# Performance work log

Measured on AMD Instinct MI355X. Metric: run time of the kernel, lower is better.

The kernel has to match this reference:

```python
import jax, jax.numpy as jnp
import numpy as np

H, KV, D, HID = 32, 2, 128, 4096
SQ, SMAX, CP, L = 1024, 4096, 3072, 4
LAYER_IDX = 0


def setup_inputs() -> dict:
    key = jax.random.key(0)
    ks = jax.random.split(key, 14)
    hidden_states = jax.random.normal(ks[0], (1, HID, 1, SQ), jnp.float32)
    # RoPE tables (values in [-1,1]; layout per forward: cos/sin act on last dim of K,
    # cos_t/sin_t are the transposed tables acting on dim -2 of Q)
    cos = jax.random.uniform(ks[1], (1, 1, SQ, D), jnp.float32, -1.0, 1.0)
    sin = jax.random.uniform(ks[2], (1, 1, SQ, D), jnp.float32, -1.0, 1.0)
    cos_t = jax.random.uniform(ks[3], (1, 1, D, SQ), jnp.float32, -1.0, 1.0)
    sin_t = jax.random.uniform(ks[4], (1, 1, D, SQ), jnp.float32, -1.0, 1.0)
    # causal mask in (kv_pos, q_pos) layout: query q sits at absolute position CP+q
    kv_pos = jnp.arange(SMAX)[:, None]
    q_pos = jnp.arange(SQ)[None, :]
    attention_mask = jnp.where(kv_pos <= CP + q_pos, 0.0, -1e9).astype(jnp.float32)[None, None]
    key_cache = jax.random.normal(ks[5], (L, KV, SMAX, D), jnp.float32)
    value_cache = jax.random.normal(ks[6], (L, KV, SMAX, D), jnp.float32)
    s = 0.02
    wq = jax.random.normal(ks[7], (H * D, HID), jnp.float32) * s
    bq = jax.random.normal(ks[8], (H * D,), jnp.float32) * s
    wk = jax.random.normal(ks[9], (KV * D, HID), jnp.float32) * s
    bk = jax.random.normal(ks[10], (KV * D,), jnp.float32) * s
    wv = jax.random.normal(ks[11], (KV * D, HID), jnp.float32) * s
    bv = jax.random.normal(ks[12], (KV * D,), jnp.float32) * s
    wo = jax.random.normal(ks[13], (HID, H * D), jnp.float32) * s
    return dict(hidden_states=hidden_states, cos=cos, sin=sin, cos_t=cos_t, sin_t=sin_t,
                attention_mask=attention_mask, key_cache=key_cache, value_cache=value_cache,
                wq=wq, bq=bq, wk=wk, bk=bk, wv=wv, bv=bv, wo=wo, cache_position=CP)


def _rotate_half(x, axis):
    x1, x2 = jnp.split(x, 2, axis=axis)
    return jnp.concatenate([-x2, x1], axis=axis)


def reference(hidden_states, cos, sin, cos_t, sin_t, attention_mask,
              key_cache, value_cache, wq, bq, wk, bk, wv, bv, wo, cache_position):
    cp = int(cache_position)
    # 1x1-conv projections == matmul over channel dim; hidden_states (1, HID, 1, SQ)
    q = jnp.einsum('oi,bihs->bohs', wq, hidden_states) + bq[None, :, None, None]
    k = jnp.einsum('oi,bihs->bohs', wk, hidden_states) + bk[None, :, None, None]
    v = jnp.einsum('oi,bihs->bohs', wv, hidden_states) + bv[None, :, None, None]
    q = q.reshape(1, H, D, SQ)                      # (1, H, D, Sq)
    k = k.reshape(1, KV, D, SQ).swapaxes(2, 3)      # (1, KV, Sq, D)
    v = v.reshape(1, KV, D, SQ).swapaxes(2, 3)      # (1, KV, Sq, D)
    # split-half RoPE: q rotated along dim -2 (head_dim axis), k along dim -1
    q = q * cos_t + _rotate_half(q, -2) * sin_t
    k = k * cos + _rotate_half(k, -1) * sin
    # scatter into KV cache at [layer_idx, :, cp:cp+SQ]
    kc = key_cache.at[LAYER_IDX, :, cp:cp + SQ, :].set(k[0])
    vc = value_cache.at[LAYER_IDX, :, cp:cp + SQ, :].set(v[0])
    kl = kc[LAYER_IDX]   # (KV, Smax, D)
    vl = vc[LAYER_IDX]   # (KV, Smax, D)
    qg = q.reshape(KV, H // KV, D, SQ)  # group G=H/KV query heads per kv head
    # K @ Q per kv-head group, softmax over kv positions (axis=2)
    attn = jnp.einsum('ksd,kgdq->kgsq', kl, qg) / jnp.sqrt(jnp.float32(D))
    attn = attn + attention_mask[0]     # broadcast (1, Smax, Sq) over (KV, G, Smax, Sq)
    attn = jax.nn.softmax(attn, axis=2)
    out = jnp.einsum('kgsq,ksd->kgqd', attn, vl)    # (KV, G, Sq, D)
    out = out.reshape(1, H, SQ, D).swapaxes(2, 3).reshape(1, H * D, 1, SQ)
    out = jnp.einsum('oi,bihs->bohs', wo, out)      # (1, HID, 1, Sq)
    return out
```

## Files before the change

### kernel.cpp

```cpp
#include <hip/hip_runtime.h>
#include <stdint.h>

#define H_    32
#define KV_   2
#define D_    128
#define HID_  4096
#define SQ_   1024
#define SMAX_ 4096

typedef unsigned short u16;
typedef __attribute__((ext_vector_type(8))) short bf16x8;
typedef __attribute__((ext_vector_type(8))) unsigned short u16x8;
typedef __attribute__((ext_vector_type(4))) float f32x4;

#define MFMA16(a, b, c) __builtin_amdgcn_mfma_f32_16x16x32_bf16(a, b, c, 0, 0, 0)

__device__ __forceinline__ u16 f2bf(float f) {
  unsigned u = __float_as_uint(f);
  u += 0x7fffu + ((u >> 16) & 1u);
  return (u16)(u >> 16);
}
__device__ __forceinline__ float bf2f(u16 u) {
  return __uint_as_float(((unsigned)u) << 16);
}
__device__ __forceinline__ float exp2_fast(float x) {
  float r;
  asm("v_exp_f32 %0, %1" : "=v"(r) : "v"(x));
  return r;
}
__device__ __forceinline__ unsigned cvt_pk_bf16(float lo, float hi) {
  unsigned r;
  asm("v_cvt_pk_bf16_f32 %0, %1, %2" : "=v"(r) : "v"(lo), "v"(hi));
  return r;
}

__device__ __forceinline__ void gl_lds16(const void* g, void* l) {
  __builtin_amdgcn_global_load_lds(
      (const __attribute__((address_space(1))) unsigned int*)g,
      (__attribute__((address_space(3))) unsigned int*)l, 16, 0, 0);
}

__global__ __launch_bounds__(256) void k_ht(const float* __restrict__ hs,
                                            u16* __restrict__ ht) {
  __shared__ float tl[64][65];
  const int i0 = blockIdx.x << 6, s0 = blockIdx.y << 6;
  const int tid = threadIdx.x;
  {
    const int r = tid >> 2, c = (tid & 3) << 4;
    const float* p = hs + (i0 + r) * SQ_ + s0 + c;
    float4 a = *(const float4*)p;
    float4 b = *(const float4*)(p + 4);
    float4 cc = *(const float4*)(p + 8);
    float4 d = *(const float4*)(p + 12);
    float* q = &tl[r][c];
    q[0] = a.x; q[1] = a.y; q[2] = a.z; q[3] = a.w;
    q[4] = b.x; q[5] = b.y; q[6] = b.z; q[7] = b.w;
    q[8] = cc.x; q[9] = cc.y; q[10] = cc.z; q[11] = cc.w;
    q[12] = d.x; q[13] = d.y; q[14] = d.z; q[15] = d.w;
  }
  __syncthreads();
  {
    const int sr = tid >> 2, c = (tid & 3) << 4;
    u16x8 o0, o1;
#pragma unroll
    for (int j = 0; j < 8; ++j) o0[j] = f2bf(tl[c + j][sr]);
#pragma unroll
    for (int j = 0; j < 8; ++j) o1[j] = f2bf(tl[c + 8 + j][sr]);
    u16* q = ht + (s0 + sr) * HID_ + i0 + c;
    *(u16x8*)q = o0;
    *(u16x8*)(q + 8) = o1;
  }
}

__global__ __launch_bounds__(256) void k_wconv4(const float* __restrict__ s0,
                                                const float* __restrict__ s1,
                                                const float* __restrict__ s2,
                                                const float* __restrict__ s3,
                                                u16* __restrict__ dbase) {
  const int N0 = (H_ * D_ * HID_) / 8;
  const int N1 = (KV_ * D_ * HID_) / 8;
  const int NT = N0 + 2 * N1 + N0;
  const int stride = gridDim.x << 8;
  for (int i = (blockIdx.x << 8) + threadIdx.x; i < NT; i += stride) {
    const float* s;
    int j;
    if (i < N0) { s = s0; j = i; }
    else if (i < N0 + N1) { s = s1; j = i - N0; }
    else if (i < N0 + 2 * N1) { s = s2; j = i - N0 - N1; }
    else { s = s3; j = i - N0 - 2 * N1; }
    const float4 a = ((const float4*)s)[2 * j];
    const float4 b = ((const float4*)s)[2 * j + 1];
    u16x8 o;
    o[0] = f2bf(a.x); o[1] = f2bf(a.y); o[2] = f2bf(a.z); o[3] = f2bf(a.w);
    o[4] = f2bf(b.x); o[5] = f2bf(b.y); o[6] = f2bf(b.z); o[7] = f2bf(b.w);
    ((u16x8*)dbase)[i] = o;
  }
}

template <int OUTMODE, bool SWZ>
__global__ __launch_bounds__(256, 2) void k_gemm_bf(const u16* __restrict__ A,
                                                    const float* __restrict__ bias,
                                                    const u16* __restrict__ B,
                                                    void* __restrict__ Cout,
                                                    const int* __restrict__ cpp,
                                                    int ldc,
                                                    const float* __restrict__ bk2,
                                                    const float* __restrict__ bv2,
                                                    u16* __restrict__ knr2,
                                                    u16* __restrict__ vt2) {
  __shared__ u16 a_t[2][64 * 64];
  __shared__ u16 b_t[2][128 * 64];
  int nx, my;
  if (SWZ) {
    const int bid = blockIdx.x;
    const int xcd = bid & 7, t = bid >> 3;
    nx = t & 7;
    my = ((t >> 3) << 3) | xcd;
  } else {
    nx = blockIdx.x;
    my = blockIdx.y;
  }
  const int n0 = nx << 7, m0 = my << 6;
  const int tid = threadIdx.x, wid = tid >> 6, lane = tid & 63;
  const int l15 = lane & 15, l4 = lane >> 4;
  const int wn = wid << 5;
  const f32x4 z4 = {0.f, 0.f, 0.f, 0.f};
  f32x4 acc[4][2];
#pragma unroll
  for (int i = 0; i < 4; ++i)
#pragma unroll
    for (int j = 0; j < 2; ++j) acc[i][j] = z4;

  const int lr8 = lane >> 3, sl = lane & 7;
  const char* sp[6];
  u16* dp[6];
  int stp[6];
#pragma unroll
  for (int j = 0; j < 6; ++j) {
    const int L = wid * 6 + j;
    const bool isA = (L < 8);
    const int Lr = isA ? L : (L - 8);
    const int row = (Lr << 3) + lr8;
    const int cs = sl ^ (row & 7);
    const size_t grow = isA ? (size_t)(m0 + row) : (size_t)(n0 + row);
    sp[j] = (const char*)((isA ? A : B) + grow * HID_) + (cs << 4);
    dp[j] = (isA ? &a_t[0][0] : &b_t[0][0]) + (Lr << 9);
    stp[j] = isA ? 4096 : 8192;
  }
#define GSTAGE(buf, kt)                                     \
  {                                                         \
    _Pragma("unroll") for (int j = 0; j < 6; ++j)           \
        gl_lds16(sp[j] + ((size_t)(kt) << 7),               \
                 dp[j] + ((buf) ? stp[j] : 0));             \
  }

  GSTAGE(0, 0);
  __syncthreads();
  int cur = 0;
  for (int kt = 0; kt < HID_ / 64; ++kt) {
    if (kt + 1 < HID_ / 64) GSTAGE(cur ^ 1, kt + 1);
#pragma unroll
    for (int kk = 0; kk < 2; ++kk) {
      bf16x8 af[4], bfr[2];
#pragma unroll
      for (int mf = 0; mf < 4; ++mf) {
        const int row = mf * 16 + l15;
        const int slt = ((kk << 2) + l4) ^ (row & 7);
        af[mf] = *(const bf16x8*)((const char*)&a_t[cur][0] + (row << 7) + (slt << 4));
      }
#pragma unroll
      for (int nf = 0; nf < 2; ++nf) {
        const int row = wn + nf * 16 + l15;
        const int slt = ((kk << 2) + l4) ^ (row & 7);
        bfr[nf] = *(const bf16x8*)((const char*)&b_t[cur][0] + (row << 7) + (slt << 4));
      }
#pragma unroll
      for (int nf = 0; nf < 2; ++nf)
#pragma unroll
        for (int mf = 0; mf < 4; ++mf) acc[mf][nf] = MFMA16(af[mf], bfr[nf], acc[mf][nf]);
    }
    __syncthreads();
    cur ^= 1;
  }
#undef GSTAGE

  if (OUTMODE == 3) {
    const int cp = cpp[0];
#pragma unroll
    for (int mf = 0; mf < 4; ++mf) {
#pragma unroll
      for (int r = 0; r < 4; ++r) {
        const int m = m0 + mf * 16 + (l4 << 2) + r;
        float bi;
        u16* dst;
        if (m < 4096) { bi = bias[m]; dst = (u16*)Cout + (size_t)m * SQ_; }
        else if (m < 4352) { bi = bk2[m - 4096]; dst = knr2 + (size_t)(m - 4096) * SQ_; }
        else { bi = bv2[m - 4352]; dst = vt2 + (size_t)(m - 4352) * SMAX_ + cp; }
#pragma unroll
        for (int nf = 0; nf < 2; ++nf) {
          const int n = n0 + wn + nf * 16 + l15;
          dst[n] = f2bf(acc[mf][nf][r] + bi);
        }
      }
    }
  } else {
#pragma unroll
    for (int mf = 0; mf < 4; ++mf) {
#pragma unroll
      for (int r = 0; r < 4; ++r) {
        const int m = m0 + mf * 16 + (l4 << 2) + r;
        const float bi = bias ? bias[m] : 0.f;
#pragma unroll
        for (int nf = 0; nf < 2; ++nf) {
          const int n = n0 + wn + nf * 16 + l15;
          const float v = acc[mf][nf][r] + bi;
          if (OUTMODE == 2)
            ((float*)Cout)[(size_t)m * ldc + n] = v;
          else
            ((u16*)Cout)[(size_t)m * ldc + n] = f2bf(v);
        }
      }
    }
  }
}

template <int OUTMODE>
__global__ __launch_bounds__(256) void k_gemm_f32A(const float* __restrict__ A,
                                                   const float* __restrict__ bias,
                                                   const u16* __restrict__ B,
                                                   void* __restrict__ Cout,
                                                   const int* __restrict__ cpp,
                                                   int ldc) {
  __shared__ u16 a_t[128 * 32];
  __shared__ u16 b_t[128 * 32];
  const int n0 = blockIdx.x << 7, m0 = blockIdx.y << 7;
  const int tid = threadIdx.x;
  const int wid = tid >> 6, lane = tid & 63;
  const int l15 = lane & 15, l4 = lane >> 4;
  const int wm = (wid >> 1) * 64, wn = (wid & 1) * 64;
  const f32x4 z4 = {0.f, 0.f, 0.f, 0.f};
  f32x4 acc[4][4];
#pragma unroll
  for (int i = 0; i < 4; ++i)
#pragma unroll
    for (int j = 0; j < 4; ++j) acc[i][j] = z4;
  const int arow = tid >> 1, ac = (tid & 1) << 4;
  const float* Ap = A + (size_t)(m0 + arow) * HID_ + ac;
  const u16* Bp = B + (size_t)(n0 + arow) * HID_ + ac;
  for (int kt = 0; kt < HID_ / 32; ++kt) {
    float4 f0 = *(const float4*)(Ap);
    float4 f1 = *(const float4*)(Ap + 4);
    float4 f2 = *(const float4*)(Ap + 8);
    float4 f3 = *(const float4*)(Ap + 12);
    uint4 b0 = *(const uint4*)(Bp);
    uint4 b1 = *(const uint4*)(Bp + 8);
    Ap += 32;
    Bp += 32;
    u16x8 ua0, ua1;
    ua0[0] = f2bf(f0.x); ua0[1] = f2bf(f0.y); ua0[2] = f2bf(f0.z); ua0[3] = f2bf(f0.w);
    ua0[4] = f2bf(f1.x); ua0[5] = f2bf(f1.y); ua0[6] = f2bf(f1.z); ua0[7] = f2bf(f1.w);
    ua1[0] = f2bf(f2.x); ua1[1] = f2bf(f2.y); ua1[2] = f2bf(f2.z); ua1[3] = f2bf(f2.w);
    ua1[4] = f2bf(f3.x); ua1[5] = f2bf(f3.y); ua1[6] = f2bf(f3.z); ua1[7] = f2bf(f3.w);
    __syncthreads();
    *(u16x8*)&a_t[arow * 32 + ac] = ua0;
    *(u16x8*)&a_t[arow * 32 + ac + 8] = ua1;
    *(uint4*)&b_t[arow * 32 + ac] = b0;
    *(uint4*)&b_t[arow * 32 + ac + 8] = b1;
    __syncthreads();
    bf16x8 af[4];
#pragma unroll
    for (int mf = 0; mf < 4; ++mf)
      af[mf] = *(const bf16x8*)&a_t[(wm + mf * 16 + l15) * 32 + l4 * 8];
#pragma unroll
    for (int nf = 0; nf < 4; ++nf) {
      bf16x8 bfr = *(const bf16x8*)&b_t[(wn + nf * 16 + l15) * 32 + l4 * 8];
#pragma unroll
      for (int mf = 0; mf < 4; ++mf) acc[mf][nf] = MFMA16(af[mf], bfr, acc[mf][nf]);
    }
  }
  const int coff = (OUTMODE == 1) ? cpp[0] : 0;
#pragma unroll
  for (int mf = 0; mf < 4; ++mf) {
#pragma unroll
    for (int r = 0; r < 4; ++r) {
      const int m = m0 + wm + mf * 16 + l4 * 4 + r;
      const float bi = bias ? bias[m] : 0.f;
#pragma unroll
      for (int nf = 0; nf < 4; ++nf) {
        const int n = n0 + wn + nf * 16 + l15;
        const float v = acc[mf][nf][r] + bi;
        if (OUTMODE == 2)
          ((float*)Cout)[(size_t)m * ldc + n] = v;
        else
          ((u16*)Cout)[(size_t)m * ldc + n + coff] = f2bf(v);
      }
    }
  }
}

__global__ __launch_bounds__(256) void k_rope_q(const u16* __restrict__ qnr,
                                                const float* __restrict__ cost,
                                                const float* __restrict__ sint,
                                                u16* __restrict__ Qr) {
  __shared__ u16 qt[128 * 64];
  __shared__ float ct[128 * 64];
  __shared__ float st[128 * 64];
  const int s0 = blockIdx.x << 6, h = blockIdx.y;
  const int tid = threadIdx.x;
  {
    const int r = tid >> 1, c = (tid & 1) << 5;
    const u16* p = qnr + (h * 128 + r) * SQ_ + s0 + c;
#pragma unroll
    for (int j = 0; j < 4; ++j) *(uint4*)&qt[r * 64 + c + j * 8] = *(const uint4*)(p + j * 8);
    const float* cpr = cost + r * SQ_ + s0 + c;
    const float* spr = sint + r * SQ_ + s0 + c;
#pragma unroll
    for (int j = 0; j < 8; ++j) {
      *(float4*)&ct[r * 64 + c + j * 4] = *(const float4*)(cpr + j * 4);
      *(float4*)&st[r * 64 + c + j * 4] = *(const float4*)(spr + j * 4);
    }
  }
  __syncthreads();
  const int sl = tid >> 2, d0 = (tid & 3) << 5;
  u16* op = Qr + (((h << 10) + s0 + sl) << 7) + d0;
#pragma unroll
  for (int g = 0; g < 4; ++g) {
    u16x8 o;
#pragma unroll
    for (int j = 0; j < 8; ++j) {
      const int d = d0 + g * 8 + j;
      const float v = bf2f(qt[d * 64 + sl]);
      const float vp = bf2f(qt[(d ^ 64) * 64 + sl]);
      const float sgn = (d < 64) ? -1.f : 1.f;
      o[j] = f2bf(v * ct[d * 64 + sl] + sgn * vp * st[d * 64 + sl]);
    }
    *(u16x8*)(op + g * 8) = o;
  }
}

__global__ __launch_bounds__(256) void k_rope_k(const u16* __restrict__ knr,
                                                const float* __restrict__ cosp,
                                                const float* __restrict__ sinp,
                                                const int* __restrict__ cpp,
                                                u16* __restrict__ kful) {
  __shared__ u16 kt_[128 * 64];
  const int s0 = blockIdx.x << 6, kk = blockIdx.y;
  const int cp = cpp[0];
  const int tid = threadIdx.x;
  {
    const int r = tid >> 1, c = (tid & 1) << 5;
    const u16* p = knr + (kk * 128 + r) * SQ_ + s0 + c;
#pragma unroll
    for (int j = 0; j < 4; ++j) *(uint4*)&kt_[r * 64 + c + j * 8] = *(const uint4*)(p + j * 8);
  }
  __syncthreads();
  const int sl = tid >> 2, d0 = (tid & 3) << 5;
  const int s = s0 + sl;
  const float* crow = cosp + s * D_;
  const float* srow = sinp + s * D_;
  u16* op = kful + ((kk * SMAX_ + cp + s) << 7) + d0;
#pragma unroll
  for (int g = 0; g < 4; ++g) {
    u16x8 o;
#pragma unroll
    for (int j = 0; j < 8; ++j) {
      const int d = d0 + g * 8 + j;
      const float v = bf2f(kt_[d * 64 + sl]);
      const float vp = bf2f(kt_[(d ^ 64) * 64 + sl]);
      const float sgn = (d < 64) ? -1.f : 1.f;
      o[j] = f2bf(v * crow[d] + sgn * vp * srow[d]);
    }
    *(u16x8*)(op + g * 8) = o;
  }
}

__global__ __launch_bounds__(256) void k_prefk(const float* __restrict__ kc,
                                               const int* __restrict__ cpp,
                                               u16* __restrict__ kful) {
  const int cp = cpp[0];
  const int idx = (blockIdx.x << 8) + threadIdx.x;
  const int base = idx << 3;
  const int s = (base >> 7) & (SMAX_ - 1);
  if (s >= cp) return;
  const float* p = kc + base;
  float4 a = *(const float4*)p;
  float4 b = *(const float4*)(p + 4);
  u16x8 o;
  o[0] = f2bf(a.x); o[1] = f2bf(a.y); o[2] = f2bf(a.z); o[3] = f2bf(a.w);
  o[4] = f2bf(b.x); o[5] = f2bf(b.y); o[6] = f2bf(b.z); o[7] = f2bf(b.w);
  *(u16x8*)(kful + base) = o;
}

__global__ __launch_bounds__(256) void k_prefvt(const float* __restrict__ vc,
                                                const int* __restrict__ cpp,
                                                u16* __restrict__ vt) {
  const int cp = cpp[0];
  const int s0 = blockIdx.x << 6, d0 = blockIdx.y << 6, kk = blockIdx.z;
  if (s0 >= cp) return;
  __shared__ float tl[64][65];
  const int tid = threadIdx.x;
  {
    const int r = tid >> 2, c = (tid & 3) << 4;
    if (s0 + r < cp) {
      const float* p = vc + ((kk * SMAX_ + s0 + r) << 7) + d0 + c;
#pragma unroll
      for (int j = 0; j < 4; ++j) {
        float4 v = *(const float4*)(p + j * 4);
        tl[r][c + j * 4 + 0] = v.x;
        tl[r][c + j * 4 + 1] = v.y;
        tl[r][c + j * 4 + 2] = v.z;
        tl[r][c + j * 4 + 3] = v.w;
      }
    }
  }
  __syncthreads();
  const int dl = tid >> 2, c = (tid & 3) << 4;
  u16* op = vt + (kk * D_ + d0 + dl) * SMAX_ + s0 + c;
  if (s0 + c + 15 < cp) {
    u16x8 o0, o1;
#pragma unroll
    for (int j = 0; j < 8; ++j) o0[j] = f2bf(tl[c + j][dl]);
#pragma unroll
    for (int j = 0; j < 8; ++j) o1[j] = f2bf(tl[c + 8 + j][dl]);
    *(u16x8*)op = o0;
    *(u16x8*)(op + 8) = o1;
  } else {
#pragma unroll
    for (int j = 0; j < 16; ++j)
      if (s0 + c + j < cp) op[j] = f2bf(tl[c + j][dl]);
  }
}

__device__ __forceinline__ void attn_stageK4(const char* KfB, int kv0, u16* kbuf,
                                             int wid, int lane) {
  const int kcb = (lane & 15) << 4;
#pragma unroll
  for (int j = 0; j < 4; ++j) {
    const int L = (wid << 2) + j;
    const int row = (L << 2) + (lane >> 4);
    gl_lds16(KfB + (((size_t)(kv0 + row)) << 8) + (kcb ^ ((row & 7) << 4)),
             kbuf + (L << 9));
  }
}
__device__ __forceinline__ void attn_stageV4(const char* VtB, int kv0, u16* vbuf,
                                             int wid, int lane) {
  const int vcb = (lane & 7) << 4;
#pragma unroll
  for (int j = 0; j < 4; ++j) {
    const int L = (wid << 2) + j;
    const int row = (L << 3) + (lane >> 3);
    gl_lds16(VtB + ((((size_t)row * SMAX_) + kv0) << 1) + (vcb ^ ((row & 7) << 4)),
             vbuf + (L << 9));
  }
}

#define SOFTMAX_G(g, sarr)                                               \
  {                                                                      \
    const int lim = cp + qrow_base + (g << 4) + l15;                     \
    if ((kv0 + 63) > (cp + qrow_base + (g << 4))) {                      \
      _Pragma("unroll") for (int nf = 0; nf < 4; ++nf)                   \
          _Pragma("unroll") for (int r = 0; r < 4; ++r)                  \
          if (kv0 + nf * 16 + (l4 << 2) + r > lim) sarr[nf][r] = -8e9f;  \
    }                                                                    \
    float t4[4];                                                         \
    _Pragma("unroll") for (int nf = 0; nf < 4; ++nf)                     \
        t4[nf] = fmaxf(fmaxf(sarr[nf][0], sarr[nf][1]),                  \
                       fmaxf(sarr[nf][2], sarr[nf][3]));                 \
    float ml = fmaxf(fmaxf(t4[0], t4[1]), fmaxf(t4[2], t4[3])) * SC2;    \
    ml = fmaxf(ml, __shfl_xor(ml, 16));                                  \
    ml = fmaxf(ml, __shfl_xor(ml, 32));                                  \
    const bool need = !__all(ml <= mrun[g] + 11.54f);                    \
    const float mnew = need ? fmaxf(ml, mrun[g]) : mrun[g];              \
    const float nm = -mnew;                                              \
    float rs = 0.f;                                                      \
    _Pragma("unroll") for (int nf = 0; nf < 4; ++nf) {                   \
      const float p0 = exp2_fast(fmaf(sarr[nf][0], SC2, nm));            \
      const float p1 = exp2_fast(fmaf(sarr[nf][1], SC2, nm));            \
      const float p2 = exp2_fast(fmaf(sarr[nf][2], SC2, nm));            \
      const float p3 = exp2_fast(fmaf(sarr[nf][3], SC2, nm));            \
      rs += (p0 + p1) + (p2 + p3);                                       \
      uint2 w;                                                           \
      w.x = cvt_pk_bf16(p0, p1);                                         \
      w.y = cvt_pk_bf16(p2, p3);                                         \
      const unsigned byte = (unsigned)(((((g << 4) + l15) << 7) +        \
          (nf << 5) + (l4 << 3)) ^ ((l15 & 7) << 4));                    \
      *(uint2*)(pl + byte) = w;                                          \
    }                                                                    \
    rs += __shfl_xor(rs, 16);                                            \
    rs += __shfl_xor(rs, 32);                                            \
    if (need) {                                                          \
      const float sf = exp2_fast(mrun[g] - mnew);                        \
      lrun[g] = lrun[g] * sf + rs;                                       \
      mrun[g] = mnew;                                                    \
      float sfr[4];                                                      \
      _Pragma("unroll") for (int r = 0; r < 4; ++r)                      \
          sfr[r] = __shfl(sf, (l4 << 2) + r);                            \
      _Pragma("unroll") for (int nf = 0; nf < 8; ++nf)                   \
          _Pragma("unroll") for (int r = 0; r < 4; ++r)                  \
          oacc[g][nf][r] *= sfr[r];                                      \
    } else {                                                             \
      lrun[g] += rs;                                                     \
    }                                                                    \
  }

template <int SPLIT>
__global__ __launch_bounds__(256, 2) void k_attn(const u16* __restrict__ Q,
                                                 const u16* __restrict__ Kf,
                                                 const u16* __restrict__ Vt,
                                                 const int* __restrict__ cpp,
                                                 u16* __restrict__ Ob,
                                                 float* __restrict__ Opart,
                                                 float* __restrict__ Ml) {
  __shared__ u16 Kb[2][8192];
  __shared__ u16 Vb[2][8192];
  __shared__ u16 Pl[4][2048];
  int h, qb, ch;
  if (SPLIT) {
    const int bid = blockIdx.x;
    const int xcd = bid & 7, s = bid >> 3;
    h = ((xcd >> 2) << 4) | (xcd & 3) | ((s & 3) << 2);
    qb = (s >> 2) & 7;
    ch = s >> 5;
  } else {
    h = blockIdx.x;
    qb = blockIdx.y;
    ch = 0;
  }
  const int cp = cpp[0];
  const int kk = h >> 4;
  const int tid = threadIdx.x, wid = tid >> 6, lane = tid & 63;
  const int l15 = lane & 15, l4 = lane >> 4;
  const int qrow_base = (qb << 7) + (wid << 5);
  char* pl = (char*)&Pl[wid][0];

  bf16x8 aq[2][4];
#pragma unroll
  for (int g = 0; g < 2; ++g)
#pragma unroll
    for (int ks = 0; ks < 4; ++ks)
      aq[g][ks] = *(const bf16x8*)&Q[(((size_t)(h << 10) + qrow_base + (g << 4) + l15) << 7) +
                                     ks * 32 + (l4 << 3)];

  const f32x4 z4 = {0.f, 0.f, 0.f, 0.f};
  f32x4 oacc[2][8];
  float mrun[2], lrun[2];
#pragma unroll
  for (int g = 0; g < 2; ++g) {
#pragma unroll
    for (int nf = 0; nf < 8; ++nf) oacc[g][nf] = z4;
    mrun[g] = -1e30f;
    lrun[g] = 0.f;
  }

  const int ntf0 = ((cp + (qb << 7) + 127) >> 6) + 1;
  const int ntf = ntf0 < (SMAX_ >> 6) ? ntf0 : (SMAX_ >> 6);
  const int t0 = (SPLIT && ch) ? 32 : 0;
  const int t1 = (SPLIT && !ch) ? 32 : ntf;
  const float SC2 = 0.12751879523568785f;

  const char* KfB = (const char*)Kf + ((size_t)kk * SMAX_ << 8);
  const char* VtB = (const char*)Vt + ((size_t)kk << 20);

  attn_stageK4(KfB, t0 << 6, Kb[0], wid, lane);
  attn_stageV4(VtB, t0 << 6, Vb[0], wid, lane);
  int cur = 0;

  for (int kt = t0; kt < t1; ++kt) {
    const int kv0 = kt << 6;
    if (kt + 1 < t1) {
      attn_stageK4(KfB, kv0 + 64, Kb[cur ^ 1], wid, lane);
      attn_stageV4(VtB, kv0 + 64, Vb[cur ^ 1], wid, lane);
      asm volatile("s_waitcnt vmcnt(8)" ::: "memory");
    } else {
      asm volatile("s_waitcnt vmcnt(0)" ::: "memory");
    }
    __builtin_amdgcn_sched_barrier(0);
    __builtin_amdgcn_s_barrier();
    __builtin_amdgcn_sched_barrier(0);

    const char* kb = (const char*)Kb[cur];
    const char* vb = (const char*)Vb[cur];
    f32x4 s0[4], s1[4];
#pragma unroll
    for (int nf = 0; nf < 4; ++nf) { s0[nf] = z4; s1[nf] = z4; }
#pragma unroll
    for (int ks = 0; ks < 4; ++ks) {
#pragma unroll
      for (int nf = 0; nf < 4; ++nf) {
        const int rk = nf * 16 + l15;
        bf16x8 bk = *(const bf16x8*)(kb + (((rk << 8) + (ks << 6) + (l4 << 4)) ^ ((rk & 7) << 4)));
        s0[nf] = MFMA16(bk, aq[0][ks], s0[nf]);
        s1[nf] = MFMA16(bk, aq[1][ks], s1[nf]);
      }
    }
    SOFTMAX_G(0, s0)
    SOFTMAX_G(1, s1)
    bf16x8 ap[2][2];
#pragma unroll
    for (int g = 0; g < 2; ++g)
#pragma unroll
      for (int k2 = 0; k2 < 2; ++k2) {
        const unsigned byte = (unsigned)(((((g << 4) + l15) << 7) + (k2 << 6) + (l4 << 4)) ^
                                         ((l15 & 7) << 4));
        ap[g][k2] = *(const bf16x8*)(pl + byte);
      }
#pragma unroll
    for (int nf = 0; nf < 8; ++nf) {
#pragma unroll
      for (int k2 = 0; k2 < 2; ++k2) {
        const int rv = nf * 16 + l15;
        bf16x8 bv = *(const bf16x8*)(vb + (((rv << 7) + (k2 << 6) + (l4 << 4)) ^ ((rv & 7) << 4)));
        oacc[0][nf] = MFMA16(ap[0][k2], bv, oacc[0][nf]);
        oacc[1][nf] = MFMA16(ap[1][k2], bv, oacc[1][nf]);
      }
    }
    __builtin_amdgcn_sched_barrier(0);
    __builtin_amdgcn_s_barrier();
    __builtin_amdgcn_sched_barrier(0);
    cur ^= 1;
  }

  float lq[2][4], mq[2][4];
#pragma unroll
  for (int g = 0; g < 2; ++g)
#pragma unroll
    for (int r = 0; r < 4; ++r) {
      lq[g][r] = __shfl(lrun[g], (l4 << 2) + r);
      mq[g][r] = __shfl(mrun[g], (l4 << 2) + r);
    }
  if (SPLIT) {
    float* Obase = Opart + ((((size_t)ch << 5) + h) << 17);
#pragma unroll
    for (int g = 0; g < 2; ++g)
#pragma unroll
      for (int r = 0; r < 4; ++r) {
        const int row = qrow_base + (g << 4) + (l4 << 2) + r;
        float* op = Obase + ((size_t)row << 7);
#pragma unroll
        for (int nf = 0; nf < 8; ++nf) op[nf * 16 + l15] = oacc[g][nf][r];
        if (l15 == 0) {
          float* mlp = Ml + ((((((size_t)ch << 5) + h) << 10) + row) << 1);
          mlp[0] = mq[g][r];
          mlp[1] = lq[g][r];
        }
      }
  } else {
#pragma unroll
    for (int g = 0; g < 2; ++g)
#pragma unroll
      for (int r = 0; r < 4; ++r) {
        const float inv = 1.f / lq[g][r];
        const int qrow = qrow_base + (g << 4) + (l4 << 2) + r;
#pragma unroll
        for (int nf = 0; nf < 8; ++nf)
          Ob[((size_t)qrow << 12) + (h << 7) + nf * 16 + l15] = f2bf(oacc[g][nf][r] * inv);
      }
  }
}

__global__ __launch_bounds__(256) void k_merge(const float* __restrict__ Opart,
                                               const float* __restrict__ Ml,
                                               u16* __restrict__ Ob) {
  const int h = blockIdx.x, qb = blockIdx.y;
  const int tid = threadIdx.x;
  const int row = (qb << 6) + (tid >> 2);
  const int d0 = (tid & 3) << 5;
  const size_t r0 = ((size_t)h << 10) + row;
  const size_t r1 = r0 + ((size_t)32 << 10);
  const float m0 = Ml[2 * r0], l0 = Ml[2 * r0 + 1];
  const float m1 = Ml[2 * r1], l1 = Ml[2 * r1 + 1];
  const float mm = fmaxf(m0, m1);
  const float w0 = exp2_fast(m0 - mm), w1 = exp2_fast(m1 - mm);
  const float inv = 1.f / (w0 * l0 + w1 * l1);
  const float a0 = w0 * inv, a1 = w1 * inv;
  const float* p0 = Opart + (r0 << 7) + d0;
  const float* p1 = Opart + (r1 << 7) + d0;
  u16* ob = Ob + (((size_t)row) << 12) + (h << 7) + d0;
#pragma unroll
  for (int g = 0; g < 4; ++g) {
    float4 u = *(const float4*)(p0 + g * 8);
    float4 v = *(const float4*)(p0 + g * 8 + 4);
    float4 x = *(const float4*)(p1 + g * 8);
    float4 y = *(const float4*)(p1 + g * 8 + 4);
    u16x8 o;
    o[0] = f2bf(a0 * u.x + a1 * x.x);
    o[1] = f2bf(a0 * u.y + a1 * x.y);
    o[2] = f2bf(a0 * u.z + a1 * x.z);
    o[3] = f2bf(a0 * u.w + a1 * x.w);
    o[4] = f2bf(a0 * v.x + a1 * y.x);
    o[5] = f2bf(a0 * v.y + a1 * y.y);
    o[6] = f2bf(a0 * v.z + a1 * y.z);
    o[7] = f2bf(a0 * v.w + a1 * y.w);
    *(u16x8*)(ob + g * 8) = o;
  }
}

extern "C" void kernel_launch(void* const* d_in, const int* in_sizes, int n_in,
                              void* d_out, int out_size, void* d_ws, size_t ws_size,
                              hipStream_t stream) {
  const float* hs    = (const float*)d_in[0];
  const float* cosp  = (const float*)d_in[1];
  const float* sinp  = (const float*)d_in[2];
  const float* cost  = (const float*)d_in[3];
  const float* sint  = (const float*)d_in[4];
  const float* kcache = (const float*)d_in[6];
  const float* vcache = (const float*)d_in[7];
  const float* wq = (const float*)d_in[8];
  const float* bq = (const float*)d_in[9];
  const float* wk = (const float*)d_in[10];
  const float* bk = (const float*)d_in[11];
  const float* wv = (const float*)d_in[12];
  const float* bv = (const float*)d_in[13];
  const float* wo = (const float*)d_in[14];
  const int* cpp = (const int*)d_in[15];

  char* ws = (char*)d_ws;
  u16* ht   = (u16*)(ws);
  u16* qnr  = (u16*)(ws + 8388608);
  u16* Qr   = (u16*)(ws + 16777216);
  u16* knr  = (u16*)(ws + 25165824);
  u16* kful = (u16*)(ws + 25690112);
  u16* vt   = (u16*)(ws + 27787264);
  u16* Ob   = (u16*)(ws + 29884416);

  const size_t WOFF  = 38273024;
  const size_t SZ_WQ = (size_t)H_ * D_ * HID_ * 2;
  const size_t SZ_WK = (size_t)KV_ * D_ * HID_ * 2;
  const size_t SZ_WO = (size_t)HID_ * H_ * D_ * 2;
  const size_t OPOFF = WOFF + SZ_WQ + 2 * SZ_WK + SZ_WO;
  const size_t SZ_OP = (size_t)2 * 32 * 1024 * 128 * 4;
  const size_t MLOFF = OPOFF + SZ_OP;
  const size_t SZ_ML = (size_t)2 * 32 * 1024 * 2 * 4;
  const bool pre = ws_size >= OPOFF;
  const bool splitok = pre && ws_size >= MLOFF + SZ_ML;

  k_ht<<<dim3(64, 16), 256, 0, stream>>>(hs, ht);
  if (pre) {
    u16* wqb = (u16*)(ws + WOFF);
    u16* wkb = (u16*)(ws + WOFF + SZ_WQ);
    u16* wvb = (u16*)(ws + WOFF + SZ_WQ + SZ_WK);
    u16* wob = (u16*)(ws + WOFF + SZ_WQ + 2 * SZ_WK);
    float* Opart = (float*)(ws + OPOFF);
    float* Ml    = (float*)(ws + MLOFF);
    k_wconv4<<<2048, 256, 0, stream>>>(wq, wk, wv, wo, wqb);
    k_gemm_bf<3, true><<<576, 256, 0, stream>>>(wqb, bq, ht, (void*)qnr, cpp, SQ_,
                                                bk, bv, knr, vt);
    k_rope_q<<<dim3(16, 32), 256, 0, stream>>>(qnr, cost, sint, Qr);
    k_rope_k<<<dim3(16, 2), 256, 0, stream>>>(knr, cosp, sinp, cpp, kful);
    k_prefk<<<dim3(512), 256, 0, stream>>>(kcache, cpp, kful);
    k_prefvt<<<dim3(64, 2, 2), 256, 0, stream>>>(vcache, cpp, vt);
    if (splitok) {
      k_attn<1><<<512, 256, 0, stream>>>(Qr, kful, vt, cpp, Ob, Opart, Ml);
      k_merge<<<dim3(32, 16), 256, 0, stream>>>(Opart, Ml, Ob);
    } else {
      k_attn<0><<<dim3(32, 8), 256, 0, stream>>>(Qr, kful, vt, cpp, Ob, nullptr, nullptr);
    }
    k_gemm_bf<2, true><<<512, 256, 0, stream>>>(wob, nullptr, Ob, d_out, nullptr, SQ_,
                                                nullptr, nullptr, nullptr, nullptr);
  } else {
    k_gemm_f32A<0><<<dim3(8, 32), 256, 0, stream>>>(wq, bq, ht, (void*)qnr, nullptr, SQ_);
    k_gemm_f32A<0><<<dim3(8, 2), 256, 0, stream>>>(wk, bk, ht, (void*)knr, nullptr, SQ_);
    k_gemm_f32A<1><<<dim3(8, 2), 256, 0, stream>>>(wv, bv, ht, (void*)vt, cpp, SMAX_);
    k_rope_q<<<dim3(16, 32), 256, 0, stream>>>(qnr, cost, sint, Qr);
    k_rope_k<<<dim3(16, 2), 256, 0, stream>>>(knr, cosp, sinp, cpp, kful);
    k_prefk<<<dim3(512), 256, 0, stream>>>(kcache, cpp, kful);
    k_prefvt<<<dim3(64, 2, 2), 256, 0, stream>>>(vcache, cpp, vt);
    k_attn<0><<<dim3(32, 8), 256, 0, stream>>>(Qr, kful, vt, cpp, Ob, nullptr, nullptr);
    k_gemm_f32A<2><<<dim3(8, 32), 256, 0, stream>>>(wo, nullptr, Ob, d_out, nullptr, SQ_);
  }
  (void)in_sizes; (void)n_in; (void)out_size; (void)ws_size;
}
```

Baseline: 274.2 us.

## Fuse fp32-to-bf16 weight conversion into the projection GEMM LDS pipeline

Drops the separate kernel that converted wq/wk/wv/wo to bf16 each call. The GEMM now streams fp32 weight tiles straight into LDS through direct global-to-LDS loads and packs them to bf16 while reading MFMA fragments. This removes a full read-and-write pass over about 100 MB of weights and one launch. In exchange the GEMM reads twice the A-operand bytes, uses twice the A-tile LDS and adds conversion ALU work in the inner loop. The old fallback path for small workspaces is also removed.

```diff
diff --git a/kernel.cpp b/kernel.cpp
--- a/kernel.cpp
+++ b/kernel.cpp
@@ -72,44 +72,16 @@
   }
 }
 
-__global__ __launch_bounds__(256) void k_wconv4(const float* __restrict__ s0,
-                                                const float* __restrict__ s1,
-                                                const float* __restrict__ s2,
-                                                const float* __restrict__ s3,
-                                                u16* __restrict__ dbase) {
-  const int N0 = (H_ * D_ * HID_) / 8;
-  const int N1 = (KV_ * D_ * HID_) / 8;
-  const int NT = N0 + 2 * N1 + N0;
-  const int stride = gridDim.x << 8;
-  for (int i = (blockIdx.x << 8) + threadIdx.x; i < NT; i += stride) {
-    const float* s;
-    int j;
-    if (i < N0) { s = s0; j = i; }
-    else if (i < N0 + N1) { s = s1; j = i - N0; }
-    else if (i < N0 + 2 * N1) { s = s2; j = i - N0 - N1; }
-    else { s = s3; j = i - N0 - 2 * N1; }
-    const float4 a = ((const float4*)s)[2 * j];
-    const float4 b = ((const float4*)s)[2 * j + 1];
-    u16x8 o;
-    o[0] = f2bf(a.x); o[1] = f2bf(a.y); o[2] = f2bf(a.z); o[3] = f2bf(a.w);
-    o[4] = f2bf(b.x); o[5] = f2bf(b.y); o[6] = f2bf(b.z); o[7] = f2bf(b.w);
-    ((u16x8*)dbase)[i] = o;
-  }
-}
-
 template <int OUTMODE, bool SWZ>
-__global__ __launch_bounds__(256, 2) void k_gemm_bf(const u16* __restrict__ A,
-                                                    const float* __restrict__ bias,
-                                                    const u16* __restrict__ B,
-                                                    void* __restrict__ Cout,
-                                                    const int* __restrict__ cpp,
-                                                    int ldc,
-                                                    const float* __restrict__ bk2,
-                                                    const float* __restrict__ bv2,
-                                                    u16* __restrict__ knr2,
-                                                    u16* __restrict__ vt2) {
-  __shared__ u16 a_t[2][64 * 64];
-  __shared__ u16 b_t[2][128 * 64];
+__global__ __launch_bounds__(256, 2) void k_gemm_f32(
+    const float* __restrict__ Aq, const float* __restrict__ Ak,
+    const float* __restrict__ Av, const float* __restrict__ bias,
+    const u16* __restrict__ B, void* __restrict__ Cout,
+    const int* __restrict__ cpp, const float* __restrict__ bk2,
+    const float* __restrict__ bv2, u16* __restrict__ knr2,
+    u16* __restrict__ vt2) {
+  __shared__ float a_t[2][64 * 64];
+  __shared__ u16   b_t[2][128 * 64];
   int nx, my;
   if (SWZ) {
     const int bid = blockIdx.x;
@@ -131,42 +103,69 @@
 #pragma unroll
     for (int j = 0; j < 2; ++j) acc[i][j] = z4;
 
-  const int lr8 = lane >> 3, sl = lane & 7;
-  const char* sp[6];
-  u16* dp[6];
-  int stp[6];
-#pragma unroll
-  for (int j = 0; j < 6; ++j) {
-    const int L = wid * 6 + j;
-    const bool isA = (L < 8);
-    const int Lr = isA ? L : (L - 8);
-    const int row = (Lr << 3) + lr8;
-    const int cs = sl ^ (row & 7);
-    const size_t grow = isA ? (size_t)(m0 + row) : (size_t)(n0 + row);
-    sp[j] = (const char*)((isA ? A : B) + grow * HID_) + (cs << 4);
-    dp[j] = (isA ? &a_t[0][0] : &b_t[0][0]) + (Lr << 9);
-    stp[j] = isA ? 4096 : 8192;
-  }
-#define GSTAGE(buf, kt)                                     \
-  {                                                         \
-    _Pragma("unroll") for (int j = 0; j < 6; ++j)           \
-        gl_lds16(sp[j] + ((size_t)(kt) << 7),               \
-                 dp[j] + ((buf) ? stp[j] : 0));             \
-  }
-
-  GSTAGE(0, 0);
+  const char* spA[4];
+  float* dpA[4];
+#pragma unroll
+  for (int j = 0; j < 4; ++j) {
+    const int L = (wid << 2) + j;
+    const int row = (L << 2) + (lane >> 4);
+    const int cs = (lane & 15) ^ (row & 7);
+    const int gr = m0 + row;
+    const float* base;
+    if (OUTMODE == 3) {
+      base = (gr < 4096) ? Aq + (size_t)gr * HID_
+           : (gr < 4352) ? Ak + (size_t)(gr - 4096) * HID_
+                         : Av + (size_t)(gr - 4352) * HID_;
+    } else {
+      base = Aq + (size_t)gr * HID_;
+    }
+    spA[j] = (const char*)base + (cs << 4);
+    dpA[j] = &a_t[0][0] + (L << 8);
+  }
+  const char* spB[4];
+  u16* dpB[4];
+#pragma unroll
+  for (int j = 0; j < 4; ++j) {
+    const int L = (wid << 2) + j;
+    const int row = (L << 3) + (lane >> 3);
+    const int cs = (lane & 7) ^ (row & 7);
+    spB[j] = (const char*)(B + (size_t)(n0 + row) * HID_) + (cs << 4);
+    dpB[j] = &b_t[0][0] + (L << 9);
+  }
+#define GSTG(buf, kt)                                          \
+  {                                                            \
+    _Pragma("unroll") for (int j = 0; j < 4; ++j)              \
+        gl_lds16(spA[j] + ((size_t)(kt) << 8),                 \
+                 dpA[j] + ((buf) ? 4096 : 0));                 \
+    _Pragma("unroll") for (int j = 0; j < 4; ++j)              \
+        gl_lds16(spB[j] + ((size_t)(kt) << 7),                 \
+                 dpB[j] + ((buf) ? 8192 : 0));                 \
+  }
+
+  GSTG(0, 0);
   __syncthreads();
   int cur = 0;
-  for (int kt = 0; kt < HID_ / 64; ++kt) {
-    if (kt + 1 < HID_ / 64) GSTAGE(cur ^ 1, kt + 1);
+  const int NT = HID_ / 64;
+  for (int kt = 0; kt < NT; ++kt) {
+    if (kt + 1 < NT) GSTG(cur ^ 1, kt + 1);
 #pragma unroll
     for (int kk = 0; kk < 2; ++kk) {
       bf16x8 af[4], bfr[2];
 #pragma unroll
       for (int mf = 0; mf < 4; ++mf) {
         const int row = mf * 16 + l15;
-        const int slt = ((kk << 2) + l4) ^ (row & 7);
-        af[mf] = *(const bf16x8*)((const char*)&a_t[cur][0] + (row << 7) + (slt << 4));
+        const int rs = row & 7;
+        const int s0 = ((kk << 3) + (l4 << 1)) ^ rs;
+        const int s1 = ((kk << 3) + (l4 << 1) + 1) ^ rs;
+        const char* aB = (const char*)&a_t[cur][0] + (row << 8);
+        const float4 fa = *(const float4*)(aB + (s0 << 4));
+        const float4 fb = *(const float4*)(aB + (s1 << 4));
+        union { uint4 u; bf16x8 v; } c;
+        c.u.x = cvt_pk_bf16(fa.x, fa.y);
+        c.u.y = cvt_pk_bf16(fa.z, fa.w);
+        c.u.z = cvt_pk_bf16(fb.x, fb.y);
+        c.u.w = cvt_pk_bf16(fb.z, fb.w);
+        af[mf] = c.v;
       }
 #pragma unroll
       for (int nf = 0; nf < 2; ++nf) {
@@ -182,7 +181,7 @@
     __syncthreads();
     cur ^= 1;
   }
-#undef GSTAGE
+#undef GSTG
 
   if (OUTMODE == 3) {
     const int cp = cpp[0];
@@ -209,90 +208,11 @@
 #pragma unroll
       for (int r = 0; r < 4; ++r) {
         const int m = m0 + mf * 16 + (l4 << 2) + r;
-        const float bi = bias ? bias[m] : 0.f;
 #pragma unroll
         for (int nf = 0; nf < 2; ++nf) {
           const int n = n0 + wn + nf * 16 + l15;
-          const float v = acc[mf][nf][r] + bi;
-          if (OUTMODE == 2)
-            ((float*)Cout)[(size_t)m * ldc + n] = v;
-          else
-            ((u16*)Cout)[(size_t)m * ldc + n] = f2bf(v);
+          ((float*)Cout)[(size_t)m * SQ_ + n] = acc[mf][nf][r];
         }
-      }
-    }
-  }
-}
-
-template <int OUTMODE>
-__global__ __launch_bounds__(256) void k_gemm_f32A(const float* __restrict__ A,
-                                                   const float* __restrict__ bias,
-                                                   const u16* __restrict__ B,
-                                                   void* __restrict__ Cout,
-                                                   const int* __restrict__ cpp,
-                                                   int ldc) {
-  __shared__ u16 a_t[128 * 32];
-  __shared__ u16 b_t[128 * 32];
-  const int n0 = blockIdx.x << 7, m0 = blockIdx.y << 7;
-  const int tid = threadIdx.x;
-  const int wid = tid >> 6, lane = tid & 63;
-  const int l15 = lane & 15, l4 = lane >> 4;
-  const int wm = (wid >> 1) * 64, wn = (wid & 1) * 64;
-  const f32x4 z4 = {0.f, 0.f, 0.f, 0.f};
-  f32x4 acc[4][4];
-#pragma unroll
-  for (int i = 0; i < 4; ++i)
-#pragma unroll
-    for (int j = 0; j < 4; ++j) acc[i][j] = z4;
-  const int arow = tid >> 1, ac = (tid & 1) << 4;
-  const float* Ap = A + (size_t)(m0 + arow) * HID_ + ac;
-  const u16* Bp = B + (size_t)(n0 + arow) * HID_ + ac;
-  for (int kt = 0; kt < HID_ / 32; ++kt) {
-    float4 f0 = *(const float4*)(Ap);
-    float4 f1 = *(const float4*)(Ap + 4);
-    float4 f2 = *(const float4*)(Ap + 8);
-    float4 f3 = *(const float4*)(Ap + 12);
-    uint4 b0 = *(const uint4*)(Bp);
-    uint4 b1 = *(const uint4*)(Bp + 8);
-    Ap += 32;
-    Bp += 32;
-    u16x8 ua0, ua1;
-    ua0[0] = f2bf(f0.x); ua0[1] = f2bf(f0.y); ua0[2] = f2bf(f0.z); ua0[3] = f2bf(f0.w);
-    ua0[4] = f2bf(f1.x); ua0[5] = f2bf(f1.y); ua0[6] = f2bf(f1.z); ua0[7] = f2bf(f1.w);
-    ua1[0] = f2bf(f2.x); ua1[1] = f2bf(f2.y); ua1[2] = f2bf(f2.z); ua1[3] = f2bf(f2.w);
-    ua1[4] = f2bf(f3.x); ua1[5] = f2bf(f3.y); ua1[6] = f2bf(f3.z); ua1[7] = f2bf(f3.w);
-    __syncthreads();
-    *(u16x8*)&a_t[arow * 32 + ac] = ua0;
-    *(u16x8*)&a_t[arow * 32 + ac + 8] = ua1;
-    *(uint4*)&b_t[arow * 32 + ac] = b0;
-    *(uint4*)&b_t[arow * 32 + ac + 8] = b1;
-    __syncthreads();
-    bf16x8 af[4];
-#pragma unroll
-    for (int mf = 0; mf < 4; ++mf)
-      af[mf] = *(const bf16x8*)&a_t[(wm + mf * 16 + l15) * 32 + l4 * 8];
-#pragma unroll
-    for (int nf = 0; nf < 4; ++nf) {
-      bf16x8 bfr = *(const bf16x8*)&b_t[(wn + nf * 16 + l15) * 32 + l4 * 8];
-#pragma unroll
-      for (int mf = 0; mf < 4; ++mf) acc[mf][nf] = MFMA16(af[mf], bfr, acc[mf][nf]);
-    }
-  }
-  const int coff = (OUTMODE == 1) ? cpp[0] : 0;
-#pragma unroll
-  for (int mf = 0; mf < 4; ++mf) {
-#pragma unroll
-    for (int r = 0; r < 4; ++r) {
-      const int m = m0 + wm + mf * 16 + l4 * 4 + r;
-      const float bi = bias ? bias[m] : 0.f;
-#pragma unroll
-      for (int nf = 0; nf < 4; ++nf) {
-        const int n = n0 + wn + nf * 16 + l15;
-        const float v = acc[mf][nf][r] + bi;
-        if (OUTMODE == 2)
-          ((float*)Cout)[(size_t)m * ldc + n] = v;
-        else
-          ((u16*)Cout)[(size_t)m * ldc + n + coff] = f2bf(v);
       }
     }
   }
@@ -723,50 +643,29 @@
   u16* vt   = (u16*)(ws + 27787264);
   u16* Ob   = (u16*)(ws + 29884416);
 
-  const size_t WOFF  = 38273024;
-  const size_t SZ_WQ = (size_t)H_ * D_ * HID_ * 2;
-  const size_t SZ_WK = (size_t)KV_ * D_ * HID_ * 2;
-  const size_t SZ_WO = (size_t)HID_ * H_ * D_ * 2;
-  const size_t OPOFF = WOFF + SZ_WQ + 2 * SZ_WK + SZ_WO;
+  const size_t OPOFF = 113770496;
   const size_t SZ_OP = (size_t)2 * 32 * 1024 * 128 * 4;
   const size_t MLOFF = OPOFF + SZ_OP;
   const size_t SZ_ML = (size_t)2 * 32 * 1024 * 2 * 4;
-  const bool pre = ws_size >= OPOFF;
-  const bool splitok = pre && ws_size >= MLOFF + SZ_ML;
+  const bool splitok = ws_size >= MLOFF + SZ_ML;
+  float* Opart = (float*)(ws + OPOFF);
+  float* Ml    = (float*)(ws + MLOFF);
 
   k_ht<<<dim3(64, 16), 256, 0, stream>>>(hs, ht);
-  if (pre) {
-    u16* wqb = (u16*)(ws + WOFF);
-    u16* wkb = (u16*)(ws + WOFF + SZ_WQ);
-    u16* wvb = (u16*)(ws + WOFF + SZ_WQ + SZ_WK);
-    u16* wob = (u16*)(ws + WOFF + SZ_WQ + 2 * SZ_WK);
-    float* Opart = (float*)(ws + OPOFF);
-    float* Ml    = (float*)(ws + MLOFF);
-    k_wconv4<<<2048, 256, 0, stream>>>(wq, wk, wv, wo, wqb);
-    k_gemm_bf<3, true><<<576, 256, 0, stream>>>(wqb, bq, ht, (void*)qnr, cpp, SQ_,
-                                                bk, bv, knr, vt);
-    k_rope_q<<<dim3(16, 32), 256, 0, stream>>>(qnr, cost, sint, Qr);
-    k_rope_k<<<dim3(16, 2), 256, 0, stream>>>(knr, cosp, sinp, cpp, kful);
-    k_prefk<<<dim3(512), 256, 0, stream>>>(kcache, cpp, kful);
-    k_prefvt<<<dim3(64, 2, 2), 256, 0, stream>>>(vcache, cpp, vt);
-    if (splitok) {
-      k_attn<1><<<512, 256, 0, stream>>>(Qr, kful, vt, cpp, Ob, Opart, Ml);
-      k_merge<<<dim3(32, 16), 256, 0, stream>>>(Opart, Ml, Ob);
-    } else {
-      k_attn<0><<<dim3(32, 8), 256, 0, stream>>>(Qr, kful, vt, cpp, Ob, nullptr, nullptr);
-    }
-    k_gemm_bf<2, true><<<512, 256, 0, stream>>>(wob, nullptr, Ob, d_out, nullptr, SQ_,
-                                                nullptr, nullptr, nullptr, nullptr);
+  k_gemm_f32<3, true><<<576, 256, 0, stream>>>(wq, wk, wv, bq, ht, (void*)qnr,
+                                               cpp, bk, bv, knr, vt);
+  k_rope_q<<<dim3(16, 32), 256, 0, stream>>>(qnr, cost, sint, Qr);
+  k_rope_k<<<dim3(16, 2), 256, 0, stream>>>(knr, cosp, sinp, cpp, kful);
+  k_prefk<<<dim3(512), 256, 0, stream>>>(kcache, cpp, kful);
+  k_prefvt<<<dim3(64, 2, 2), 256, 0, stream>>>(vcache, cpp, vt);
+  if (splitok) {
+    k_attn<1><<<512, 256, 0, stream>>>(Qr, kful, vt, cpp, Ob, Opart, Ml);
+    k_merge<<<dim3(32, 16), 256, 0, stream>>>(Opart, Ml, Ob);
   } else {
-    k_gemm_f32A<0><<<dim3(8, 32), 256, 0, stream>>>(wq, bq, ht, (void*)qnr, nullptr, SQ_);
-    k_gemm_f32A<0><<<dim3(8, 2), 256, 0, stream>>>(wk, bk, ht, (void*)knr, nullptr, SQ_);
-    k_gemm_f32A<1><<<dim3(8, 2), 256, 0, stream>>>(wv, bv, ht, (void*)vt, cpp, SMAX_);
-    k_rope_q<<<dim3(16, 32), 256, 0, stream>>>(qnr, cost, sint, Qr);
-    k_rope_k<<<dim3(16, 2), 256, 0, stream>>>(knr, cosp, sinp, cpp, kful);
-    k_prefk<<<dim3(512), 256, 0, stream>>>(kcache, cpp, kful);
-    k_prefvt<<<dim3(64, 2, 2), 256, 0, stream>>>(vcache, cpp, vt);
     k_attn<0><<<dim3(32, 8), 256, 0, stream>>>(Qr, kful, vt, cpp, Ob, nullptr, nullptr);
-    k_gemm_f32A<2><<<dim3(8, 32), 256, 0, stream>>>(wo, nullptr, Ob, d_out, nullptr, SQ_);
-  }
+  }
+  k_gemm_f32<2, true><<<512, 256, 0, stream>>>(wo, nullptr, nullptr, nullptr, Ob,
+                                               d_out, cpp, nullptr, nullptr,
+                                               nullptr, nullptr);
   (void)in_sizes; (void)n_in; (void)out_size; (void)ws_size;
 }
```

Result: slower. 338.4 us (+23.4%).
